# Performance work log

Hardware: AMD Instinct MI355X
Metric: run time of the kernel (lower is better)

## Reference

```python
import jax, jax.numpy as jnp
import numpy as np

B, H, I, S = 4096, 2048, 2048, 3
TAU = 1.0
LN_EPS = 1e-5
SC = 0.02  # weight init scale to keep tanh/sigmoid in a sane range


def setup_inputs() -> dict:
    key = jax.random.key(0)
    ks = jax.random.split(key, 10)
    # precomputed Gumbel(0,1) noise for gumbel_softmax (deterministic reference)
    u = jax.random.uniform(ks[3], (B, S), minval=1e-6, maxval=1.0 - 1e-6)
    gumbel = -jnp.log(-jnp.log(u))
    return {
        "x": jax.random.normal(ks[0], (B, I), dtype=jnp.float32),
        "prev_master_h": jax.random.normal(ks[1], (B, H), dtype=jnp.float32),
        "prev_sub_h": jax.random.normal(ks[2], (S, B, H), dtype=jnp.float32),
        "gumbel": gumbel.astype(jnp.float32),
        "W_ih": jax.random.normal(ks[4], (S, H, I), dtype=jnp.float32) * SC,
        "W_hh": jax.random.normal(ks[5], (S, H, H), dtype=jnp.float32) * SC,
        "b_ih": jnp.zeros((S, H), dtype=jnp.float32),
        "b_hh": jnp.zeros((S, H), dtype=jnp.float32),
        "gate_W": jax.random.normal(ks[6], (S, H), dtype=jnp.float32) * SC,
        "gate_b": jnp.zeros((S,), dtype=jnp.float32),
        "fusion_W": jax.random.normal(ks[7], (H, H), dtype=jnp.float32) * SC,
        "fusion_b": jnp.zeros((H,), dtype=jnp.float32),
        "ln_g": jnp.ones((H,), dtype=jnp.float32),
        "ln_b": jnp.zeros((H,), dtype=jnp.float32),
    }


def reference(x, prev_master_h, prev_sub_h, gumbel, W_ih, W_hh, b_ih, b_hh,
              gate_W, gate_b, fusion_W, fusion_b, ln_g, ln_b):
    # gate logits: Linear(hidden -> num_sub), torch Linear is x @ W.T + b
    logits = prev_master_h @ gate_W.T + gate_b              # [B, S]
    # hard gumbel-softmax with straight-through estimator
    y_soft = jax.nn.softmax((logits + gumbel) / TAU, axis=-1)
    y_hard = jax.nn.one_hot(jnp.argmax(y_soft, axis=-1), S, dtype=y_soft.dtype)
    gate = y_hard + y_soft - jax.lax.stop_gradient(y_soft)  # [B, S]
    # vectorized vanilla RNN sub-cells: tanh(x W_ih^T + h W_hh^T + b)
    new_sub = jnp.tanh(
        jnp.einsum('bi,shi->sbh', x, W_ih)
        + jnp.einsum('sbi,shi->sbh', prev_sub_h, W_hh)
        + b_ih[:, None, :] + b_hh[:, None, :]
    )                                                        # [S, B, H]
    # hard one-hot mixture of sub-cell states
    weighted = jnp.einsum('bs,sbh->bh', gate, new_sub)       # [B, H]
    fused = weighted @ fusion_W.T + fusion_b                 # [B, H]
    pre = prev_master_h + fused
    mu = jnp.mean(pre, axis=-1, keepdims=True)
    var = jnp.mean(jnp.square(pre - mu), axis=-1, keepdims=True)
    normed = (pre - mu) * jax.lax.rsqrt(var + LN_EPS) * ln_g + ln_b
    master_h_new = jax.nn.sigmoid(normed)
    return master_h_new, gate, new_sub
```

## Files before the change

### kernel.cpp

```cpp
#include <hip/hip_runtime.h>
#include <cstdint>
#include <cstddef>

#define B_SZ 4096
#define H_SZ 2048
#define S_SZ 3

typedef __attribute__((ext_vector_type(8))) _Float16 f16x8;
typedef __attribute__((ext_vector_type(4))) float f32x4;

__device__ __forceinline__ void glds16(const void* g, void* l) {
    __builtin_amdgcn_global_load_lds(
        (const __attribute__((address_space(1))) void*)g,
        (__attribute__((address_space(3))) void*)l, 16, 0, 0);
}

__device__ __forceinline__ float wave_red_sum(float v) {
#pragma unroll
    for (int off = 32; off > 0; off >>= 1) v += __shfl_down(v, off);
    return v;
}

__global__ __launch_bounds__(256) void cvt_f16_kernel(
    const float* __restrict__ src, _Float16* __restrict__ dst, int n4)
{
    const int i = blockIdx.x * 256 + threadIdx.x;
    if (i >= n4) return;
    const float4 v = ((const float4*)src)[i];
    _Float16 h[4];
    h[0] = (_Float16)v.x; h[1] = (_Float16)v.y;
    h[2] = (_Float16)v.z; h[3] = (_Float16)v.w;
    *(uint2*)(dst + (size_t)i * 4) = *(const uint2*)h;
}

__global__ __launch_bounds__(64) void gate_kernel(
    const float* __restrict__ prev_master, const float* __restrict__ gate_W,
    const float* __restrict__ gate_b, const float* __restrict__ gumbel,
    float* __restrict__ out_gate)
{
    const int b = blockIdx.x;
    const int lane = threadIdx.x;
    const float* row = prev_master + (size_t)b * H_SZ;
    double a0 = 0.0, a1 = 0.0, a2 = 0.0;
#pragma unroll
    for (int k = lane * 4; k < H_SZ; k += 64 * 4) {
        float4 v  = *(const float4*)(row + k);
        float4 w0 = *(const float4*)(gate_W + 0 * H_SZ + k);
        float4 w1 = *(const float4*)(gate_W + 1 * H_SZ + k);
        float4 w2 = *(const float4*)(gate_W + 2 * H_SZ + k);
        a0 += (double)v.x * w0.x + (double)v.y * w0.y + (double)v.z * w0.z + (double)v.w * w0.w;
        a1 += (double)v.x * w1.x + (double)v.y * w1.y + (double)v.z * w1.z + (double)v.w * w1.w;
        a2 += (double)v.x * w2.x + (double)v.y * w2.y + (double)v.z * w2.z + (double)v.w * w2.w;
    }
#pragma unroll
    for (int off = 32; off > 0; off >>= 1) {
        a0 += __shfl_down(a0, off);
        a1 += __shfl_down(a1, off);
        a2 += __shfl_down(a2, off);
    }
    if (lane == 0) {
        float z0 = (float)a0 + gate_b[0] + gumbel[b * 3 + 0];
        float z1 = (float)a1 + gate_b[1] + gumbel[b * 3 + 1];
        float z2 = (float)a2 + gate_b[2] + gumbel[b * 3 + 2];
        float zm = fmaxf(z0, fmaxf(z1, z2));
        float e0 = expf(z0 - zm), e1 = expf(z1 - zm), e2 = expf(z2 - zm);
        float se = e0 + e1 + e2;
        float y0 = e0 / se, y1 = e1 / se, y2 = e2 / se;
        int am = 0; float best = y0;
        if (y1 > best) { best = y1; am = 1; }
        if (y2 > best) { best = y2; am = 2; }
        float h0 = (am == 0) ? 1.0f : 0.0f;
        float h1 = (am == 1) ? 1.0f : 0.0f;
        float h2 = (am == 2) ? 1.0f : 0.0f;
        out_gate[b * 3 + 0] = (h0 + y0) - y0;
        out_gate[b * 3 + 1] = (h1 + y1) - y1;
        out_gate[b * 3 + 2] = (h2 + y2) - y2;
    }
}

template<int MODE, int NT>
__global__ __launch_bounds__(512, 2) void tile_gemm_kernel(
    const _Float16* __restrict__ A0, const _Float16* __restrict__ A1,
    const _Float16* __restrict__ W0, const _Float16* __restrict__ W1,
    const float* __restrict__ bias0, const float* __restrict__ bias1,
    const float* __restrict__ prev_master, float* __restrict__ out)
{
    __shared__ __align__(16) _Float16 lds[5 * 12288];

    const int flat = blockIdx.x;
    constexpr int QX = (MODE == 0) ? 96 : 32;
    const int L  = (flat & 7) * QX + (flat >> 3);
    const int ly = L & 31;
    const int lx = (L >> 5) & 7;
    const int s  = (MODE == 0) ? (L >> 8) : 0;
    const int am0 = ly * 128;
    const int n0  = lx * 256;

    const int tid  = threadIdx.x;
    const int lane = tid & 63;
    const int wave = tid >> 6;
    const int wm = wave >> 2;
    const int wn = wave & 3;
    const int lrow = lane & 15;
    const int fcol = ((lane >> 4) ^ ((lrow >> 1) & 3)) * 8;
    const int srow   = tid >> 2;
    const int schunk = (tid & 3) ^ ((tid >> 3) & 3);
    const int ldst   = wave << 9;

    int roa[4], rob[4];
#pragma unroll
    for (int i = 0; i < 4; ++i) {
        roa[i] = (wm * 64 + i * 16 + lrow) * 32 + fcol;
        rob[i] = 4096 + (wn * 64 + i * 16 + lrow) * 32 + fcol;
    }

    f32x4 acc[4][4] = {};
    f16x8 fAa[4], fAb[4], fBa[4], fBb[4];

    auto stage = [&](int t, int bufe) {
        int kb; const _Float16 *As, *Ws;
        if constexpr (MODE == 0) {
            kb = (t & 63) * 32;
            if (t < 64) { As = A0;                             Ws = W0 + (size_t)s * (H_SZ * 2048); }
            else        { As = A1 + (size_t)s * (B_SZ * 2048); Ws = W1 + (size_t)s * (H_SZ * 2048); }
        } else {
            kb = t * 32; As = A0; Ws = W0;
        }
        const int ko = kb + schunk * 8;
        glds16(As + (size_t)(am0 + srow)       * 2048 + ko, &lds[bufe + ldst]);
        glds16(Ws + (size_t)(n0  + srow)       * 2048 + ko, &lds[bufe + 4096 + ldst]);
        glds16(Ws + (size_t)(n0  + 128 + srow) * 2048 + ko, &lds[bufe + 8192 + ldst]);
    };

    auto read_frags = [&](int bufe, f16x8 (&fa)[4], f16x8 (&fb)[4]) {
#pragma unroll
        for (int i = 0; i < 4; ++i) {
            fa[i] = *(const f16x8*)&lds[bufe + roa[i]];
            fb[i] = *(const f16x8*)&lds[bufe + rob[i]];
        }
    };

    auto mfma16 = [&](const f16x8 (&fa)[4], const f16x8 (&fb)[4]) {
        __builtin_amdgcn_s_setprio(1);
#pragma unroll
        for (int i = 0; i < 4; ++i)
#pragma unroll
            for (int j = 0; j < 4; ++j)
                acc[i][j] = __builtin_amdgcn_mfma_f32_16x16x32_f16(fa[i], fb[j], acc[i][j], 0, 0, 0);
        __builtin_amdgcn_s_setprio(0);
    };

    auto sync_tile = [&](int u) {
        __builtin_amdgcn_sched_barrier(0);
        if (u <= NT - 5)      asm volatile("s_waitcnt vmcnt(6)" ::: "memory");
        else if (u == NT - 4) asm volatile("s_waitcnt vmcnt(3)" ::: "memory");
        else if (u == NT - 3) asm volatile("s_waitcnt vmcnt(0)" ::: "memory");
        else return;
        __builtin_amdgcn_s_barrier();
        asm volatile("" ::: "memory");
    };

    stage(0, 0); stage(1, 12288); stage(2, 24576); stage(3, 36864);
    asm volatile("s_waitcnt vmcnt(6)" ::: "memory");
    __builtin_amdgcn_s_barrier();
    asm volatile("" ::: "memory");
    read_frags(0, fAa, fAb);

    int c = 0;
    for (int t = 0; t < NT; t += 2) {
        int b1 = c + 1; if (b1 >= 5) b1 -= 5;
        int b2 = c + 2; if (b2 >= 5) b2 -= 5;
        int b4 = c + 4; if (b4 >= 5) b4 -= 5;
        if (t + 4 < NT) stage(t + 4, b4 * 12288);
        read_frags(b1 * 12288, fBa, fBb);
        mfma16(fAa, fAb);
        sync_tile(t);
        if (t + 5 < NT) stage(t + 5, c * 12288);
        if (t + 2 < NT) read_frags(b2 * 12288, fAa, fAb);
        mfma16(fBa, fBb);
        sync_tile(t + 1);
        c += 2; if (c >= 5) c -= 5;
    }

#pragma unroll
    for (int j = 0; j < 4; ++j) {
        const int n = n0 + wn * 64 + j * 16 + lrow;
        float badd;
        if constexpr (MODE == 0) badd = bias0[s * H_SZ + n] + bias1[s * H_SZ + n];
        else                     badd = bias0[n];
#pragma unroll
        for (int i = 0; i < 4; ++i) {
            const int mb = am0 + wm * 64 + i * 16 + (lane >> 4) * 4;
#pragma unroll
            for (int r = 0; r < 4; ++r) {
                const int m = mb + r;
                if constexpr (MODE == 0)
                    out[((size_t)s * B_SZ + m) * H_SZ + n] = tanhf(acc[i][j][r] + badd);
                else
                    out[(size_t)m * H_SZ + n] =
                        acc[i][j][r] + badd + prev_master[(size_t)m * H_SZ + n];
            }
        }
    }
}

__global__ __launch_bounds__(256) void weighted_kernel(
    const float* __restrict__ new_sub, const float* __restrict__ gate,
    _Float16* __restrict__ w16)
{
    const size_t p = (size_t)blockIdx.x * 256 + threadIdx.x;
    const size_t b = p / (H_SZ / 4);
    const int h4 = (int)(p % (H_SZ / 4)) * 4;
    const float g0 = gate[b * 3 + 0], g1 = gate[b * 3 + 1], g2 = gate[b * 3 + 2];
    const float4 v0 = *(const float4*)(new_sub + ((size_t)0 * B_SZ + b) * H_SZ + h4);
    const float4 v1 = *(const float4*)(new_sub + ((size_t)1 * B_SZ + b) * H_SZ + h4);
    const float4 v2 = *(const float4*)(new_sub + ((size_t)2 * B_SZ + b) * H_SZ + h4);
    _Float16 h[4];
    h[0] = (_Float16)(g0 * v0.x + g1 * v1.x + g2 * v2.x);
    h[1] = (_Float16)(g0 * v0.y + g1 * v1.y + g2 * v2.y);
    h[2] = (_Float16)(g0 * v0.z + g1 * v1.z + g2 * v2.z);
    h[3] = (_Float16)(g0 * v0.w + g1 * v1.w + g2 * v2.w);
    *(uint2*)(w16 + b * H_SZ + h4) = *(const uint2*)h;
}

__global__ __launch_bounds__(256) void ln_sigmoid_kernel(
    float* __restrict__ master, const float* __restrict__ ln_g,
    const float* __restrict__ ln_b)
{
    const int b = blockIdx.x;
    const int t = threadIdx.x;
    float* row = master + (size_t)b * H_SZ;
    float v[8];
    float4 p0 = *(const float4*)(row + t * 4);
    float4 p1 = *(const float4*)(row + 1024 + t * 4);
    v[0] = p0.x; v[1] = p0.y; v[2] = p0.z; v[3] = p0.w;
    v[4] = p1.x; v[5] = p1.y; v[6] = p1.z; v[7] = p1.w;
    float lsum = 0.f;
#pragma unroll
    for (int e = 0; e < 8; ++e) lsum += v[e];
    __shared__ float red[8];
    float wsum = wave_red_sum(lsum);
    const int lane = t & 63, wid = t >> 6;
    if (lane == 0) red[wid] = wsum;
    __syncthreads();
    const float mu = (red[0] + red[1] + red[2] + red[3]) * (1.0f / H_SZ);
    float lsq = 0.f;
#pragma unroll
    for (int e = 0; e < 8; ++e) { float d = v[e] - mu; lsq += d * d; }
    float wsq = wave_red_sum(lsq);
    if (lane == 0) red[4 + wid] = wsq;
    __syncthreads();
    const float var = (red[4] + red[5] + red[6] + red[7]) * (1.0f / H_SZ);
    const float rs = rsqrtf(var + 1e-5f);
#pragma unroll
    for (int half = 0; half < 2; ++half)
#pragma unroll
        for (int e = 0; e < 4; ++e) {
            const int col = half * 1024 + t * 4 + e;
            const float nm = (v[half * 4 + e] - mu) * rs * ln_g[col] + ln_b[col];
            row[col] = 1.0f / (1.0f + expf(-nm));
        }
}

extern "C" void kernel_launch(void* const* d_in, const int* in_sizes, int n_in,
                              void* d_out, int out_size, void* d_ws, size_t ws_size,
                              hipStream_t stream)
{
    const float* x           = (const float*)d_in[0];
    const float* prev_master = (const float*)d_in[1];
    const float* prev_sub    = (const float*)d_in[2];
    const float* gumbel      = (const float*)d_in[3];
    const float* W_ih        = (const float*)d_in[4];
    const float* W_hh        = (const float*)d_in[5];
    const float* b_ih        = (const float*)d_in[6];
    const float* b_hh        = (const float*)d_in[7];
    const float* gate_W      = (const float*)d_in[8];
    const float* gate_b      = (const float*)d_in[9];
    const float* fusion_W    = (const float*)d_in[10];
    const float* fusion_b    = (const float*)d_in[11];
    const float* ln_g        = (const float*)d_in[12];
    const float* ln_b        = (const float*)d_in[13];

    float* out = (float*)d_out;
    float* out_master  = out;
    float* out_gate    = out + (size_t)B_SZ * H_SZ;
    float* out_new_sub = out_gate + (size_t)B_SZ * S_SZ;

    _Float16* ws = (_Float16*)d_ws;
    _Float16* x16    = ws;
    _Float16* sub16  = x16   + (size_t)B_SZ * H_SZ;
    _Float16* Wih16  = sub16 + (size_t)S_SZ * B_SZ * H_SZ;
    _Float16* Whh16  = Wih16 + (size_t)S_SZ * H_SZ * H_SZ;
    _Float16* fusW16 = Whh16 + (size_t)S_SZ * H_SZ * H_SZ;
    _Float16* wtd16  = fusW16 + (size_t)H_SZ * H_SZ;

    const int n4_x   = B_SZ * H_SZ / 4;
    const int n4_sub = S_SZ * B_SZ * H_SZ / 4;
    const int n4_w   = S_SZ * H_SZ * H_SZ / 4;
    const int n4_fw  = H_SZ * H_SZ / 4;

    cvt_f16_kernel<<<n4_x / 256, 256, 0, stream>>>(x, x16, n4_x);
    cvt_f16_kernel<<<n4_sub / 256, 256, 0, stream>>>(prev_sub, sub16, n4_sub);
    cvt_f16_kernel<<<n4_w / 256, 256, 0, stream>>>(W_ih, Wih16, n4_w);
    cvt_f16_kernel<<<n4_w / 256, 256, 0, stream>>>(W_hh, Whh16, n4_w);
    cvt_f16_kernel<<<n4_fw / 256, 256, 0, stream>>>(fusion_W, fusW16, n4_fw);

    gate_kernel<<<B_SZ, 64, 0, stream>>>(prev_master, gate_W, gate_b, gumbel, out_gate);

    tile_gemm_kernel<0, 128><<<768, 512, 0, stream>>>(
        x16, sub16, Wih16, Whh16, b_ih, b_hh, nullptr, out_new_sub);

    weighted_kernel<<<(B_SZ * (H_SZ / 4)) / 256, 256, 0, stream>>>(
        out_new_sub, out_gate, wtd16);

    tile_gemm_kernel<1, 64><<<256, 512, 0, stream>>>(
        wtd16, nullptr, fusW16, nullptr, fusion_b, nullptr, prev_master, out_master);

    ln_sigmoid_kernel<<<B_SZ, 256, 0, stream>>>(out_master, ln_g, ln_b);
}
```

Measured before the change: 702.8 us.

## Restructure GEMM to 4 waves with 128x64 per-wave tiles and triple buffering

The tile GEMM now runs with 256 threads instead of 512. Each of the 4 waves computes a 128x64 slab, so it holds 8x4 accumulators and reuses A fragments across all four B fragments. The 5-stage LDS ring with software-pipelined fragment prefetch becomes a simpler 3-buffer ring with a prefetch distance of 2. The five fp16 conversion launches are merged into one kernel to cut launch overhead. The change risks higher register pressure, since 32 f32x4 accumulators compete with __launch_bounds__(256,2), and the shallower pipeline gives less latency hiding.

```diff
diff --git a/kernel.cpp b/kernel.cpp
--- a/kernel.cpp
+++ b/kernel.cpp
@@ -21,16 +21,26 @@
     return v;
 }
 
-__global__ __launch_bounds__(256) void cvt_f16_kernel(
-    const float* __restrict__ src, _Float16* __restrict__ dst, int n4)
-{
-    const int i = blockIdx.x * 256 + threadIdx.x;
-    if (i >= n4) return;
-    const float4 v = ((const float4*)src)[i];
+__global__ __launch_bounds__(256) void cvt_all_kernel(
+    const float* __restrict__ s0, const float* __restrict__ s1,
+    const float* __restrict__ s2, const float* __restrict__ s3,
+    const float* __restrict__ s4, _Float16* __restrict__ dst)
+{
+    constexpr size_t c1 = (size_t)B_SZ * H_SZ / 4;
+    constexpr size_t c2 = c1 + (size_t)S_SZ * B_SZ * H_SZ / 4;
+    constexpr size_t c3 = c2 + (size_t)S_SZ * H_SZ * H_SZ / 4;
+    constexpr size_t c4 = c3 + (size_t)S_SZ * H_SZ * H_SZ / 4;
+    const size_t i = (size_t)blockIdx.x * 256 + threadIdx.x;
+    const float* src; size_t rel;
+    if (i < c2)      { if (i < c1) { src = s0; rel = i; } else { src = s1; rel = i - c1; } }
+    else if (i < c3) { src = s2; rel = i - c2; }
+    else if (i < c4) { src = s3; rel = i - c3; }
+    else             { src = s4; rel = i - c4; }
+    const float4 v = ((const float4*)src)[rel];
     _Float16 h[4];
     h[0] = (_Float16)v.x; h[1] = (_Float16)v.y;
     h[2] = (_Float16)v.z; h[3] = (_Float16)v.w;
-    *(uint2*)(dst + (size_t)i * 4) = *(const uint2*)h;
+    *(uint2*)(dst + i * 4) = *(const uint2*)h;
 }
 
 __global__ __launch_bounds__(64) void gate_kernel(
@@ -79,13 +89,13 @@
 }
 
 template<int MODE, int NT>
-__global__ __launch_bounds__(512, 2) void tile_gemm_kernel(
+__global__ __launch_bounds__(256, 2) void tile_gemm_kernel(
     const _Float16* __restrict__ A0, const _Float16* __restrict__ A1,
     const _Float16* __restrict__ W0, const _Float16* __restrict__ W1,
     const float* __restrict__ bias0, const float* __restrict__ bias1,
     const float* __restrict__ prev_master, float* __restrict__ out)
 {
-    __shared__ __align__(16) _Float16 lds[5 * 12288];
+    __shared__ __align__(16) _Float16 lds[3 * 12288];
 
     const int flat = blockIdx.x;
     constexpr int QX = (MODE == 0) ? 96 : 32;
@@ -99,25 +109,14 @@
     const int tid  = threadIdx.x;
     const int lane = tid & 63;
     const int wave = tid >> 6;
-    const int wm = wave >> 2;
-    const int wn = wave & 3;
     const int lrow = lane & 15;
     const int fcol = ((lane >> 4) ^ ((lrow >> 1) & 3)) * 8;
-    const int srow   = tid >> 2;
-    const int schunk = (tid & 3) ^ ((tid >> 3) & 3);
-    const int ldst   = wave << 9;
-
-    int roa[4], rob[4];
-#pragma unroll
-    for (int i = 0; i < 4; ++i) {
-        roa[i] = (wm * 64 + i * 16 + lrow) * 32 + fcol;
-        rob[i] = 4096 + (wn * 64 + i * 16 + lrow) * 32 + fcol;
-    }
-
-    f32x4 acc[4][4] = {};
-    f16x8 fAa[4], fAb[4], fBa[4], fBb[4];
-
-    auto stage = [&](int t, int bufe) {
+    const int srow   = lane >> 2;
+    const int schunk = (lane & 3) ^ ((lane >> 3) & 3);
+
+    f32x4 acc[8][4] = {};
+
+    auto stage = [&](int t, int buf) {
         int kb; const _Float16 *As, *Ws;
         if constexpr (MODE == 0) {
             kb = (t & 63) * 32;
@@ -127,70 +126,64 @@
             kb = t * 32; As = A0; Ws = W0;
         }
         const int ko = kb + schunk * 8;
-        glds16(As + (size_t)(am0 + srow)       * 2048 + ko, &lds[bufe + ldst]);
-        glds16(Ws + (size_t)(n0  + srow)       * 2048 + ko, &lds[bufe + 4096 + ldst]);
-        glds16(Ws + (size_t)(n0  + 128 + srow) * 2048 + ko, &lds[bufe + 8192 + ldst]);
+        const int be = buf * 12288;
+#pragma unroll
+        for (int u = 0; u < 2; ++u) {
+            const int slot = wave + u * 4;
+            glds16(As + (size_t)(am0 + slot * 16 + srow) * 2048 + ko,
+                   &lds[be + slot * 512]);
+        }
+#pragma unroll
+        for (int u = 0; u < 4; ++u) {
+            const int slot = wave + u * 4;
+            glds16(Ws + (size_t)(n0 + slot * 16 + srow) * 2048 + ko,
+                   &lds[be + 4096 + slot * 512]);
+        }
     };
 
-    auto read_frags = [&](int bufe, f16x8 (&fa)[4], f16x8 (&fb)[4]) {
-#pragma unroll
-        for (int i = 0; i < 4; ++i) {
-            fa[i] = *(const f16x8*)&lds[bufe + roa[i]];
-            fb[i] = *(const f16x8*)&lds[bufe + rob[i]];
-        }
-    };
-
-    auto mfma16 = [&](const f16x8 (&fa)[4], const f16x8 (&fb)[4]) {
-        __builtin_amdgcn_s_setprio(1);
-#pragma unroll
-        for (int i = 0; i < 4; ++i)
-#pragma unroll
-            for (int j = 0; j < 4; ++j)
-                acc[i][j] = __builtin_amdgcn_mfma_f32_16x16x32_f16(fa[i], fb[j], acc[i][j], 0, 0, 0);
-        __builtin_amdgcn_s_setprio(0);
-    };
-
-    auto sync_tile = [&](int u) {
-        __builtin_amdgcn_sched_barrier(0);
-        if (u <= NT - 5)      asm volatile("s_waitcnt vmcnt(6)" ::: "memory");
-        else if (u == NT - 4) asm volatile("s_waitcnt vmcnt(3)" ::: "memory");
-        else if (u == NT - 3) asm volatile("s_waitcnt vmcnt(0)" ::: "memory");
-        else return;
-        __builtin_amdgcn_s_barrier();
-        asm volatile("" ::: "memory");
-    };
-
-    stage(0, 0); stage(1, 12288); stage(2, 24576); stage(3, 36864);
+    stage(0, 0); stage(1, 1);
     asm volatile("s_waitcnt vmcnt(6)" ::: "memory");
     __builtin_amdgcn_s_barrier();
     asm volatile("" ::: "memory");
-    read_frags(0, fAa, fAb);
-
-    int c = 0;
-    for (int t = 0; t < NT; t += 2) {
-        int b1 = c + 1; if (b1 >= 5) b1 -= 5;
-        int b2 = c + 2; if (b2 >= 5) b2 -= 5;
-        int b4 = c + 4; if (b4 >= 5) b4 -= 5;
-        if (t + 4 < NT) stage(t + 4, b4 * 12288);
-        read_frags(b1 * 12288, fBa, fBb);
-        mfma16(fAa, fAb);
-        sync_tile(t);
-        if (t + 5 < NT) stage(t + 5, c * 12288);
-        if (t + 2 < NT) read_frags(b2 * 12288, fAa, fAb);
-        mfma16(fBa, fBb);
-        sync_tile(t + 1);
-        c += 2; if (c >= 5) c -= 5;
+
+    int cb = 0, cs = 2;
+#pragma unroll 1
+    for (int t = 0; t < NT; ++t) {
+        if (t + 2 < NT) stage(t + 2, cs);
+        const int be = cb * 12288;
+        f16x8 af[8], bf[4];
+#pragma unroll
+        for (int i = 0; i < 8; ++i)
+            af[i] = *(const f16x8*)&lds[be + (i * 16 + lrow) * 32 + fcol];
+#pragma unroll
+        for (int j = 0; j < 4; ++j)
+            bf[j] = *(const f16x8*)&lds[be + 4096 + (wave * 64 + j * 16 + lrow) * 32 + fcol];
+        __builtin_amdgcn_s_setprio(1);
+#pragma unroll
+        for (int i = 0; i < 8; ++i)
+#pragma unroll
+            for (int j = 0; j < 4; ++j)
+                acc[i][j] = __builtin_amdgcn_mfma_f32_16x16x32_f16(af[i], bf[j], acc[i][j], 0, 0, 0);
+        __builtin_amdgcn_s_setprio(0);
+        __builtin_amdgcn_sched_barrier(0);
+        if (t < NT - 2)       asm volatile("s_waitcnt vmcnt(6)" ::: "memory");
+        else if (t == NT - 2) asm volatile("s_waitcnt vmcnt(0)" ::: "memory");
+        else break;
+        __builtin_amdgcn_s_barrier();
+        asm volatile("" ::: "memory");
+        cb = (cb == 2) ? 0 : cb + 1;
+        cs = (cs == 2) ? 0 : cs + 1;
     }
 
 #pragma unroll
     for (int j = 0; j < 4; ++j) {
-        const int n = n0 + wn * 64 + j * 16 + lrow;
+        const int n = n0 + wave * 64 + j * 16 + lrow;
         float badd;
         if constexpr (MODE == 0) badd = bias0[s * H_SZ + n] + bias1[s * H_SZ + n];
         else                     badd = bias0[n];
 #pragma unroll
-        for (int i = 0; i < 4; ++i) {
-            const int mb = am0 + wm * 64 + i * 16 + (lane >> 4) * 4;
+        for (int i = 0; i < 8; ++i) {
+            const int mb = am0 + i * 16 + (lane >> 4) * 4;
 #pragma unroll
             for (int r = 0; r < 4; ++r) {
                 const int m = mb + r;
@@ -294,26 +287,20 @@
     _Float16* fusW16 = Whh16 + (size_t)S_SZ * H_SZ * H_SZ;
     _Float16* wtd16  = fusW16 + (size_t)H_SZ * H_SZ;
 
-    const int n4_x   = B_SZ * H_SZ / 4;
-    const int n4_sub = S_SZ * B_SZ * H_SZ / 4;
-    const int n4_w   = S_SZ * H_SZ * H_SZ / 4;
-    const int n4_fw  = H_SZ * H_SZ / 4;
-
-    cvt_f16_kernel<<<n4_x / 256, 256, 0, stream>>>(x, x16, n4_x);
-    cvt_f16_kernel<<<n4_sub / 256, 256, 0, stream>>>(prev_sub, sub16, n4_sub);
-    cvt_f16_kernel<<<n4_w / 256, 256, 0, stream>>>(W_ih, Wih16, n4_w);
-    cvt_f16_kernel<<<n4_w / 256, 256, 0, stream>>>(W_hh, Whh16, n4_w);
-    cvt_f16_kernel<<<n4_fw / 256, 256, 0, stream>>>(fusion_W, fusW16, n4_fw);
+    const int n4_total = (B_SZ * H_SZ + S_SZ * B_SZ * H_SZ + 2 * S_SZ * H_SZ * H_SZ
+                          + H_SZ * H_SZ) / 4;
+    cvt_all_kernel<<<n4_total / 256, 256, 0, stream>>>(
+        x, prev_sub, W_ih, W_hh, fusion_W, ws);
 
     gate_kernel<<<B_SZ, 64, 0, stream>>>(prev_master, gate_W, gate_b, gumbel, out_gate);
 
-    tile_gemm_kernel<0, 128><<<768, 512, 0, stream>>>(
+    tile_gemm_kernel<0, 128><<<768, 256, 0, stream>>>(
         x16, sub16, Wih16, Whh16, b_ih, b_hh, nullptr, out_new_sub);
 
     weighted_kernel<<<(B_SZ * (H_SZ / 4)) / 256, 256, 0, stream>>>(
         out_new_sub, out_gate, wtd16);
 
-    tile_gemm_kernel<1, 64><<<256, 512, 0, stream>>>(
+    tile_gemm_kernel<1, 64><<<256, 256, 0, stream>>>(
         wtd16, nullptr, fusW16, nullptr, fusion_b, nullptr, prev_master, out_master);
 
     ln_sigmoid_kernel<<<B_SZ, 256, 0, stream>>>(out_master, ln_g, ln_b);
```

Result: faster. 670.0 us (-4.7%).
